# Optimization experiments

Measured on AMD Instinct MI355X. Metric: run time of the kernel, lower is better.

Reference implementation:

```python
import jax, jax.numpy as jnp
import numpy as np
import math

T, P, L, C, H, NPTS = 243, 17, 4, 128, 8, 4
DH = C // H


def _ln(x, g, b):
    m = jnp.mean(x, axis=-1, keepdims=True)
    v = jnp.mean((x - m) ** 2, axis=-1, keepdims=True)
    return (x - m) * jax.lax.rsqrt(v + 1e-5) * g + b


def _bilinear(v, grid):
    # v: [B, D, Hh, Ww]; grid: [B, Q, Pt, 2] in [-1,1], (x->W, y->H),
    # align_corners=False, zero padding (matches F.grid_sample in MSDeformAttn core)
    B, D, Hh, Ww = v.shape
    x = (grid[..., 0] + 1.0) * (Ww * 0.5) - 0.5
    y = (grid[..., 1] + 1.0) * (Hh * 0.5) - 0.5
    x0 = jnp.floor(x)
    y0 = jnp.floor(y)
    x0i = x0.astype(jnp.int32)
    y0i = y0.astype(jnp.int32)
    x1i = x0i + 1
    y1i = y0i + 1
    wx1 = x - x0
    wx0 = 1.0 - wx1
    wy1 = y - y0
    wy0 = 1.0 - wy1
    vf = v.reshape(B, D, Hh * Ww)
    Q, Pt = x.shape[1], x.shape[2]

    def gather(yi, xi):
        valid = ((yi >= 0) & (yi < Hh) & (xi >= 0) & (xi < Ww)).astype(v.dtype)
        idx = jnp.clip(yi, 0, Hh - 1) * Ww + jnp.clip(xi, 0, Ww - 1)
        g = jnp.take_along_axis(vf, idx.reshape(B, 1, Q * Pt), axis=2).reshape(B, D, Q, Pt)
        return g * valid[:, None]

    return (gather(y0i, x0i) * (wy0 * wx0)[:, None]
            + gather(y0i, x1i) * (wy0 * wx1)[:, None]
            + gather(y1i, x0i) * (wy1 * wx0)[:, None]
            + gather(y1i, x1i) * (wy1 * wx1)[:, None])  # [B, D, Q, Pt]


def _forward(x, ref_points, pe_buf, learn_pos, w_off, b_off, w_attn, b_attn,
             w_val, b_val, w_out, b_out, in_w, in_b, out_w, out_b,
             fc1_w, fc1_b, fc2_w, fc2_b, g1, be1, g2, be2, g3, be3):
    b, t, p, l, c = x.shape  # l = n_levels + 1
    Lq = t * p * L
    x0 = x[..., :1, :]
    xs = x[..., 1:, :].reshape(b, Lq, c)
    # --- subforward_self: norm_1 -> PE(query) -> MSDeformAttn ---
    xn = _ln(xs, g1, be1)
    q = (xn.reshape(b, t, p, L, c) + pe_buf + learn_pos).reshape(b, Lq, c)
    off = (q @ w_off.T + b_off).reshape(b, Lq, H, L, NPTS, 2)
    aw = jax.nn.softmax((q @ w_attn.T + b_attn).reshape(b, Lq, H, L * NPTS), axis=-1)
    aw = aw.reshape(b, Lq, H, L, NPTS)
    ref = jnp.broadcast_to(ref_points[:, :, :, None, :], (b, t, p, L, 2)).reshape(b, Lq, 2)
    normalizer = jnp.array([p, t], dtype=x.dtype)  # (W, H) per level
    loc = ref[:, :, None, None, None, :] + off / normalizer  # [b,Lq,H,L,Pt,2]
    grids = 2.0 * loc - 1.0
    val = (xn @ w_val.T + b_val).reshape(b, t, p, L, H, DH)
    v_maps = val.transpose(3, 0, 4, 5, 1, 2).reshape(L, b * H, DH, t, p)
    g = grids.transpose(3, 0, 2, 1, 4, 5).reshape(L, b * H, Lq, NPTS, 2)
    sampled = jax.vmap(_bilinear)(v_maps, g)  # [L, b*H, DH, Lq, Pt]
    aw_t = aw.transpose(3, 0, 2, 1, 4).reshape(L, b * H, 1, Lq, NPTS)
    o = jnp.sum(sampled * aw_t, axis=(0, 4))  # [b*H, DH, Lq]
    o = o.reshape(b, H, DH, Lq).transpose(0, 3, 1, 2).reshape(b, Lq, c)
    xs = (o @ w_out.T + b_out) + xs
    # --- concat level-0 back, cross (self) MHA over (p*l) tokens per frame ---
    xcat = jnp.concatenate([x0, xs.reshape(b, t, p, L, c)], axis=3).reshape(b * t, p * l, c)
    xn2 = _ln(xcat, g2, be2)
    qkv = xn2 @ in_w.T + in_b
    qh, kh, vh = jnp.split(qkv, 3, axis=-1)
    S = p * l
    qh = qh.reshape(b * t, S, H, DH)
    kh = kh.reshape(b * t, S, H, DH)
    vh = vh.reshape(b * t, S, H, DH)
    att = jax.nn.softmax(jnp.einsum('bqhd,bkhd->bhqk', qh, kh) / math.sqrt(DH), axis=-1)
    ca = jnp.einsum('bhqk,bkhd->bqhd', att, vh).reshape(b * t, S, c) @ out_w.T + out_b
    xcat = ca + xcat
    xr = xcat.reshape(b, t, p, l, c)
    # --- MLP block ---
    h = _ln(xr, g3, be3)
    h = jax.nn.gelu(h @ fc1_w.T + fc1_b, approximate=False) @ fc2_w.T + fc2_b
    return h + xr


def setup_inputs() -> dict:
    key = jax.random.key(0)
    ks = jax.random.split(key, 20)
    B = 2
    s = 0.02
    x = jax.random.normal(ks[0], (B, T, P, L + 1, C), jnp.float32)
    ref_points = jax.random.uniform(ks[1], (B, T, P, 2), dtype=jnp.float32)
    # sinusoidal PE buffer
    pos = np.arange(T, dtype=np.float32)[:, None]
    div = np.exp(np.arange(0, C, 2, dtype=np.float32) * (-math.log(10000.0) / C))
    ang = pos * div  # [T, C//2]
    pe = np.zeros((1, T, P, L, C), np.float32)
    pe[..., 0::2] = np.sin(ang)[None, :, None, None, :]
    pe[..., 1::2] = np.cos(ang)[None, :, None, None, :]
    rn = lambda k, shp: s * jax.random.normal(k, shp, jnp.float32)
    return {
        'x': x, 'ref_points': ref_points,
        'pe_buf': jnp.asarray(pe),
        'learn_pos': rn(ks[2], (1, T, P, L, C)),
        'w_off': rn(ks[3], (H * L * NPTS * 2, C)), 'b_off': rn(ks[4], (H * L * NPTS * 2,)),
        'w_attn': rn(ks[5], (H * L * NPTS, C)), 'b_attn': rn(ks[6], (H * L * NPTS,)),
        'w_val': rn(ks[7], (C, C)), 'b_val': rn(ks[8], (C,)),
        'w_out': rn(ks[9], (C, C)), 'b_out': rn(ks[10], (C,)),
        'in_w': rn(ks[11], (3 * C, C)), 'in_b': rn(ks[12], (3 * C,)),
        'out_w': rn(ks[13], (C, C)), 'out_b': rn(ks[14], (C,)),
        'fc1_w': rn(ks[15], (4 * C, C)), 'fc1_b': rn(ks[16], (4 * C,)),
        'fc2_w': rn(ks[17], (C, 4 * C)), 'fc2_b': rn(ks[18], (C,)),
        'g1': jnp.ones((C,), jnp.float32), 'be1': jnp.zeros((C,), jnp.float32),
        'g2': jnp.ones((C,), jnp.float32), 'be2': jnp.zeros((C,), jnp.float32),
        'g3': jnp.ones((C,), jnp.float32), 'be3': jnp.zeros((C,), jnp.float32),
    }


def reference(x, ref_points, pe_buf, learn_pos, w_off, b_off, w_attn, b_attn,
              w_val, b_val, w_out, b_out, in_w, in_b, out_w, out_b,
              fc1_w, fc1_b, fc2_w, fc2_b, g1, be1, g2, be2, g3, be3):
    return _forward(x, ref_points, pe_buf, learn_pos, w_off, b_off, w_attn, b_attn,
                    w_val, b_val, w_out, b_out, in_w, in_b, out_w, out_b,
                    fc1_w, fc1_b, fc2_w, fc2_b, g1, be1, g2, be2, g3, be3)
```

## Files before the change

kernel.cpp:

```cpp
#include <hip/hip_runtime.h>
#include <math.h>

#define T_ 243
#define P_ 17
#define L_ 4
#define C_ 128
#define H_ 8
#define NPTS_ 4
#define DH_ 16
#define B_ 2
#define LQ (T_*P_*L_)
#define NT1 (B_*LQ)
#define LL (L_+1)
#define S_ (P_*LL)
#define NT2 (B_*T_*P_*LL)

typedef __attribute__((ext_vector_type(8))) short short8v;
typedef __attribute__((ext_vector_type(4))) short short4v;
typedef __attribute__((ext_vector_type(4))) float float4v;

__device__ __forceinline__ unsigned short f2bf(float f){
  union { float f; unsigned u; } un; un.f = f;
  unsigned r = un.u + 0x7FFF + ((un.u >> 16) & 1);
  return (unsigned short)(r >> 16);
}
__device__ __forceinline__ float bf2f(unsigned short u){
  union { unsigned u; float f; } un; un.u = ((unsigned)u) << 16; return un.f;
}
__device__ __forceinline__ void dma16(const unsigned short* g, unsigned short* l){
  __builtin_amdgcn_global_load_lds(
      (const __attribute__((address_space(1))) void*)g,
      (__attribute__((address_space(3))) void*)l, 16, 0, 0);
}

__global__ void k_wcvt(const float* __restrict__ w0, const float* __restrict__ w1,
                       const float* __restrict__ w2, const float* __restrict__ w3,
                       const float* __restrict__ w4, const float* __restrict__ w5,
                       const float* __restrict__ w6, const float* __restrict__ w7,
                       unsigned short* __restrict__ dst){
  int i = blockIdx.x*256 + threadIdx.x;
  if (i >= 278528) return;
  float v;
  if      (i < 32768)  v = w0[i];
  else if (i < 49152)  v = w1[i-32768];
  else if (i < 65536)  v = w2[i-49152];
  else if (i < 81920)  v = w3[i-65536];
  else if (i < 131072) v = w4[i-81920];
  else if (i < 147456) v = w5[i-131072];
  else if (i < 212992) v = w6[i-147456];
  else                 v = w7[i-212992];
  dst[i] = f2bf(v);
}

__global__ __launch_bounds__(256) void k_ln1_q(
    const float* __restrict__ x, const float* __restrict__ pe,
    const float* __restrict__ lpos, const float* __restrict__ g1,
    const float* __restrict__ be1, const float* __restrict__ g2,
    const float* __restrict__ be2, unsigned short* __restrict__ xn,
    unsigned short* __restrict__ q, float* __restrict__ xcat,
    unsigned short* __restrict__ xn2) {
  int w = threadIdx.x >> 6; int lane = threadIdx.x & 63;
  int i = blockIdx.x*4 + w;
  int c = lane*2;
  if (i < NT1){
    int b = i / LQ; int r = i % LQ;
    int t = r / (P_*L_); int rp = r % (P_*L_);
    int p = rp / L_; int lv = rp % L_;
    const float* xrow = x + (((size_t)(b*T_+t)*P_ + p)*LL + 1 + lv)*C_;
    float2 v = *(const float2*)(xrow + c);
    float s1 = v.x + v.y, s2 = v.x*v.x + v.y*v.y;
    #pragma unroll
    for (int d=1; d<64; d<<=1){ s1 += __shfl_xor(s1,d); s2 += __shfl_xor(s2,d); }
    float mean = s1*(1.0f/C_);
    float var  = s2*(1.0f/C_) - mean*mean;
    float inv = rsqrtf(var + 1e-5f);
    float2 gg = *(const float2*)(g1 + c);
    float2 bb = *(const float2*)(be1 + c);
    float xn0 = (v.x - mean)*inv*gg.x + bb.x;
    float xn1 = (v.y - mean)*inv*gg.y + bb.y;
    size_t oi = (size_t)i*C_ + c;
    *(unsigned*)(xn + oi) = (unsigned)f2bf(xn0) | ((unsigned)f2bf(xn1) << 16);
    size_t pidx = (((size_t)t*P_ + p)*L_ + lv)*C_ + c;
    float2 pv = *(const float2*)(pe + pidx);
    float2 lp = *(const float2*)(lpos + pidx);
    *(unsigned*)(q + oi) = (unsigned)f2bf(xn0 + pv.x + lp.x) | ((unsigned)f2bf(xn1 + pv.y + lp.y) << 16);
  } else {
    int i0 = i - NT1;
    if (i0 >= B_*T_*P_) return;
    size_t xrow = (size_t)i0*LL;
    const float* xr = x + xrow*C_;
    float2 v = *(const float2*)(xr + c);
    float s1 = v.x + v.y, s2 = v.x*v.x + v.y*v.y;
    #pragma unroll
    for (int d=1; d<64; d<<=1){ s1 += __shfl_xor(s1,d); s2 += __shfl_xor(s2,d); }
    float mean = s1*(1.0f/C_);
    float var  = s2*(1.0f/C_) - mean*mean;
    float inv = rsqrtf(var + 1e-5f);
    float2 gg = *(const float2*)(g2 + c);
    float2 bb = *(const float2*)(be2 + c);
    *(float2*)(xcat + xrow*C_ + c) = v;
    float o0 = (v.x - mean)*inv*gg.x + bb.x;
    float o1 = (v.y - mean)*inv*gg.y + bb.y;
    *(unsigned*)(xn2 + xrow*C_ + c) = (unsigned)f2bf(o0) | ((unsigned)f2bf(o1) << 16);
  }
}

template<int K, int N, int EPI>
__global__ __launch_bounds__(256) void k_mm(
    const unsigned short* __restrict__ A, const unsigned short* __restrict__ Bw,
    const float* __restrict__ bias, const float* __restrict__ res,
    float* __restrict__ outF, unsigned short* __restrict__ outB,
    const float* __restrict__ xres, const float* __restrict__ lng,
    const float* __restrict__ lnbe, int M)
{
  constexpr int NST = K / 128;
  __shared__ unsigned short As[64*128];
  __shared__ unsigned short Bs[128*128];
  int tid = threadIdx.x;
  int lane = tid & 63;
  int w = tid >> 6;
  int lr = lane & 15, kg = lane >> 4;
  int m0 = blockIdx.x * 64;
  int n0 = blockIdx.y * 128;
  int lrow = lane >> 4;
  int lch  = lane & 15;
  float4v acc[8] = {};
  for (int st = 0; st < NST; ++st){
    int kk = st*128;
    if (st) __syncthreads();
    #pragma unroll
    for (int j = 0; j < 4; ++j){
      int rb = w*16 + j*4;
      int srcch = lch ^ ((rb + lrow) & 7);
      dma16(A + (size_t)(m0 + rb + lrow)*K + kk + srcch*8, As + rb*128);
    }
    #pragma unroll
    for (int j = 0; j < 8; ++j){
      int rb = w*32 + j*4;
      int srcch = lch ^ ((rb + lrow) & 7);
      dma16(Bw + (size_t)(n0 + rb + lrow)*K + kk + srcch*8, Bs + rb*128);
    }
    __syncthreads();
    #pragma unroll
    for (int ks = 0; ks < 4; ++ks){
      int cn = ks*4 + kg;
      int arow = w*16 + lr;
      short8v af = *(const short8v*)(As + arow*128 + ((cn ^ (arow & 7)) * 8));
      #pragma unroll
      for (int nf = 0; nf < 8; ++nf){
        int brow = nf*16 + lr;
        short8v bf = *(const short8v*)(Bs + brow*128 + ((cn ^ (brow & 7)) * 8));
        acc[nf] = __builtin_amdgcn_mfma_f32_16x16x32_bf16(af, bf, acc[nf], 0, 0, 0);
      }
    }
  }
  #pragma unroll
  for (int j = 0; j < 4; ++j){
    int gr = m0 + w*16 + kg*4 + j;
    if (gr >= M) continue;
    if (EPI == 3 || EPI == 4 || EPI == 5){
      #pragma unroll
      for (int nf = 0; nf < 8; ++nf){
        int gc = n0 + nf*16 + lr;
        float v = acc[nf][j] + bias[gc];
        if (EPI == 3) {
          outF[(size_t)gr*N + gc] = v + res[(size_t)gr*N + gc];
        } else if (EPI == 4) {
          float gv = 0.5f*v*(1.0f + erff(v*0.70710678118654752440f));
          outB[(size_t)gr*N + gc] = f2bf(gv);
        } else {
          outB[(size_t)gr*N + gc] = f2bf(v);
        }
      }
    } else {
      size_t xrow;
      if (EPI == 6){
        int b = gr / LQ; int r = gr % LQ;
        int t = r / (P_*L_); int rp = r % (P_*L_);
        int p = rp / L_; int lv = rp % L_;
        xrow = (((size_t)(b*T_+t)*P_ + p)*LL) + 1 + lv;
      } else {
        xrow = (size_t)gr;
      }
      float vals[8];
      float s = 0.f, sq = 0.f;
      #pragma unroll
      for (int nf = 0; nf < 8; ++nf){
        int gc = n0 + nf*16 + lr;
        float v = acc[nf][j] + bias[gc];
        if (EPI == 6) v += xres[xrow*C_ + gc];
        else          v += res[xrow*C_ + gc];
        vals[nf] = v; s += v; sq += v*v;
      }
      #pragma unroll
      for (int d = 1; d < 16; d <<= 1){ s += __shfl_xor(s, d); sq += __shfl_xor(sq, d); }
      float mean = s*(1.0f/128.f);
      float varr = sq*(1.0f/128.f) - mean*mean;
      float linv = rsqrtf(varr + 1e-5f);
      #pragma unroll
      for (int nf = 0; nf < 8; ++nf){
        int gc = n0 + nf*16 + lr;
        outF[xrow*C_ + gc] = vals[nf];
        float ln = (vals[nf] - mean)*linv*lng[gc] + lnbe[gc];
        outB[xrow*C_ + gc] = f2bf(ln);
      }
    }
  }
}

__global__ __launch_bounds__(256) void k_mm3(
    const unsigned short* __restrict__ Aq, const unsigned short* __restrict__ Axn,
    const unsigned short* __restrict__ Bw,
    const float* __restrict__ b_off, const float* __restrict__ b_attn,
    const float* __restrict__ b_val,
    unsigned short* __restrict__ off_b, unsigned short* __restrict__ aw_b,
    unsigned short* __restrict__ vm_b, int M)
{
  __shared__ unsigned short As[64*128];
  __shared__ unsigned short Bs[128*128];
  int tid = threadIdx.x;
  int lane = tid & 63;
  int w = tid >> 6;
  int lr = lane & 15, kg = lane >> 4;
  int m0 = blockIdx.x * 64;
  int y  = blockIdx.y;
  int n0 = y * 128;
  const unsigned short* A = (y == 3) ? Axn : Aq;
  int lrow = lane >> 4;
  int lch  = lane & 15;
  float4v acc[8] = {};
  #pragma unroll
  for (int j = 0; j < 4; ++j){
    int rb = w*16 + j*4;
    int srcch = lch ^ ((rb + lrow) & 7);
    dma16(A + (size_t)(m0 + rb + lrow)*128 + srcch*8, As + rb*128);
  }
  #pragma unroll
  for (int j = 0; j < 8; ++j){
    int rb = w*32 + j*4;
    int srcch = lch ^ ((rb + lrow) & 7);
    dma16(Bw + (size_t)(n0 + rb + lrow)*128 + srcch*8, Bs + rb*128);
  }
  __syncthreads();
  #pragma unroll
  for (int ks = 0; ks < 4; ++ks){
    int cn = ks*4 + kg;
    int arow = w*16 + lr;
    short8v af = *(const short8v*)(As + arow*128 + ((cn ^ (arow & 7)) * 8));
    #pragma unroll
    for (int nf = 0; nf < 8; ++nf){
      int brow = nf*16 + lr;
      short8v bf = *(const short8v*)(Bs + brow*128 + ((cn ^ (brow & 7)) * 8));
      acc[nf] = __builtin_amdgcn_mfma_f32_16x16x32_bf16(af, bf, acc[nf], 0, 0, 0);
    }
  }
  const float* bias = (y < 2) ? b_off : (y == 2 ? b_attn - 256 : b_val - 384);
  #pragma unroll
  for (int j = 0; j < 4; ++j){
    int gr = m0 + w*16 + kg*4 + j;
    if (gr >= M) continue;
    #pragma unroll
    for (int nf = 0; nf < 8; ++nf){
      int gc = n0 + nf*16 + lr;
      float v = acc[nf][j] + bias[gc];
      unsigned short bv = f2bf(v);
      if (y < 2)      off_b[(size_t)gr*256 + gc]       = bv;
      else if (y==2)  aw_b [(size_t)gr*128 + gc - 256] = bv;
      else            vm_b [(size_t)gr*128 + gc - 384] = bv;
    }
  }
}

__global__ __launch_bounds__(256) void k_sample(
    const unsigned short* __restrict__ off, const unsigned short* __restrict__ awl,
    const float* __restrict__ refp, const unsigned short* __restrict__ vmap,
    unsigned short* __restrict__ o){
  int gid = blockIdx.x*256 + threadIdx.x;
  if (gid >= NT1*H_) return;
  int h = gid & 7; int i = gid >> 3;
  int b = i / LQ; int r = i % LQ;
  int t = r/(P_*L_); int rp = r%(P_*L_); int p = rp/L_;
  size_t rpi = (((size_t)b*T_+t)*P_+p)*2;
  float refx = refp[rpi + 0]*P_ - 0.5f;
  float refy = refp[rpi + 1]*T_ - 0.5f;

  float offv[32];
  {
    const short8v* op8 = (const short8v*)(off + (size_t)i*256 + h*32);
    #pragma unroll
    for (int s=0;s<4;++s){ short8v v = op8[s];
      #pragma unroll
      for (int j=0;j<8;++j) offv[s*8+j] = bf2f((unsigned short)v[j]); }
  }
  float awv[16];
  {
    const short8v* ap8 = (const short8v*)(awl + (size_t)i*128 + h*16);
    #pragma unroll
    for (int s=0;s<2;++s){ short8v v = ap8[s];
      #pragma unroll
      for (int j=0;j<8;++j) awv[s*8+j] = bf2f((unsigned short)v[j]); }
  }
  float m = awv[0];
  #pragma unroll
  for (int k=1;k<16;++k) m = fmaxf(m, awv[k]);
  float sum = 0.f;
  #pragma unroll
  for (int k=0;k<16;++k){ awv[k] = __expf(awv[k]-m); sum += awv[k]; }
  float inv = 1.f/sum;
  #pragma unroll
  for (int k=0;k<16;++k) awv[k] *= inv;

  float acc[16];
  #pragma unroll
  for (int d=0;d<16;++d) acc[d]=0.f;

  #pragma unroll
  for (int lv=0; lv<L_; ++lv){
    const unsigned short* vlv = vmap + ((size_t)b*LQ + lv)*128 + h*16;
    #pragma unroll
    for (int pt=0; pt<NPTS_; ++pt){
      float px = refx + offv[(lv*4+pt)*2+0];
      float py = refy + offv[(lv*4+pt)*2+1];
      float w  = awv[lv*4+pt];
      float fx = floorf(px), fy = floorf(py);
      int x0 = (int)fx, y0 = (int)fy;
      float wx1 = px - fx, wx0 = 1.f - wx1;
      float wy1 = py - fy, wy0 = 1.f - wy1;
      float cw[4] = {w*wy0*wx0, w*wy0*wx1, w*wy1*wx0, w*wy1*wx1};
      int ys[4] = {y0, y0, y0+1, y0+1};
      int xs[4] = {x0, x0+1, x0, x0+1};
      #pragma unroll
      for (int cidx=0; cidx<4; ++cidx){
        int yy = ys[cidx], xx = xs[cidx];
        if (yy>=0 && yy<T_ && xx>=0 && xx<P_){
          const short8v* vp = (const short8v*)(vlv + (size_t)(yy*P_ + xx)*(L_*128));
          short8v v0 = vp[0], v1 = vp[1];
          float wgt = cw[cidx];
          #pragma unroll
          for (int d=0;d<8;++d){
            acc[d]   = fmaf(wgt, bf2f((unsigned short)v0[d]), acc[d]);
            acc[8+d] = fmaf(wgt, bf2f((unsigned short)v1[d]), acc[8+d]);
          }
        }
      }
    }
  }
  short8v o0, o1;
  #pragma unroll
  for (int d=0;d<8;++d){ o0[d] = (short)f2bf(acc[d]); o1[d] = (short)f2bf(acc[8+d]); }
  short8v* op = (short8v*)(o + (size_t)i*C_ + h*DH_);
  op[0] = o0; op[1] = o1;
}

#define AT6_WAVE 6976
__global__ __launch_bounds__(128) void k_attn6(const unsigned short* __restrict__ qkv,
                                               unsigned short* __restrict__ ca){
  __shared__ unsigned short alds[2*AT6_WAVE];
  int w = threadIdx.x >> 6; int lane = threadIdx.x & 63;
  int bt = blockIdx.x >> 2; int hp = blockIdx.x & 3;
  int h = hp*2 + w;
  unsigned short* Kb  = alds + w*AT6_WAVE;
  unsigned short* Vb  = Kb + 1920;
  unsigned short* Pb0 = Kb + 3648;
  unsigned short* Pb1 = Kb + 5312;
  const unsigned short* base = qkv + (size_t)bt*85*384 + h*16;
  for (int idx = lane; idx < 192; idx += 64){
    int s = idx >> 1; int d0 = (idx & 1)*8;
    short8v kv = {}, vv = {};
    if (s < 85){
      const unsigned short* rp = base + (size_t)s*384 + d0;
      kv = *(const short8v*)(rp + 128);
      vv = *(const short8v*)(rp + 256);
    }
    *(short8v*)(Kb + s*20 + d0) = kv;
    #pragma unroll
    for (int j=0;j<8;++j) Vb[(d0+j)*108 + s] = (unsigned short)vv[j];
  }
  __syncthreads();
  int g = lane >> 4; int li = lane & 15;
  const short8v zero8 = {};
  short8v qf0 = zero8, qf1 = zero8;
  if (g < 2){
    if (li < 85) qf0 = *(const short8v*)(base + (size_t)li*384 + g*8);
    int q1i = 16 + li;
    if (q1i < 85) qf1 = *(const short8v*)(base + (size_t)q1i*384 + g*8);
  }
  #pragma unroll 1
  for (int qp = 0; qp < 3; ++qp){
    short8v qn0 = zero8, qn1 = zero8;
    if (qp < 2 && g < 2){
      int a = (qp+1)*32 + li, b2 = a + 16;
      if (a  < 85) qn0 = *(const short8v*)(base + (size_t)a *384 + g*8);
      if (b2 < 85) qn1 = *(const short8v*)(base + (size_t)b2*384 + g*8);
    }
    float4v sc0[6], sc1[6];
    __builtin_amdgcn_s_setprio(1);
    #pragma unroll
    for (int kt = 0; kt < 6; ++kt){
      short8v kf = zero8;
      if (g < 2) kf = *(const short8v*)(Kb + (kt*16 + li)*20 + g*8);
      float4v z = {};
      sc0[kt] = __builtin_amdgcn_mfma_f32_16x16x32_bf16(kf, qf0, z, 0, 0, 0);
      sc1[kt] = __builtin_amdgcn_mfma_f32_16x16x32_bf16(kf, qf1, z, 0, 0, 0);
    }
    __builtin_amdgcn_s_setprio(0);
    float sum0 = 0.f, sum1 = 0.f;
    #pragma unroll
    for (int kt = 0; kt < 6; ++kt){
      short4v p0, p1;
      #pragma unroll
      for (int j = 0; j < 4; ++j){
        bool msk = (kt == 5 && (g*4 + j) >= 5);
        float e0 = msk ? 0.f : __expf(sc0[kt][j]*0.25f);
        float e1 = msk ? 0.f : __expf(sc1[kt][j]*0.25f);
        sum0 += e0; p0[j] = (short)f2bf(e0);
        sum1 += e1; p1[j] = (short)f2bf(e1);
      }
      *(short4v*)(Pb0 + li*104 + kt*16 + g*4) = p0;
      *(short4v*)(Pb1 + li*104 + kt*16 + g*4) = p1;
    }
    sum0 += __shfl_xor(sum0, 16); sum1 += __shfl_xor(sum1, 16);
    sum0 += __shfl_xor(sum0, 32); sum1 += __shfl_xor(sum1, 32);
    float inv0 = 1.f/sum0, inv1 = 1.f/sum1;
    float4v o0 = {}, o1 = {};
    __builtin_amdgcn_s_setprio(1);
    #pragma unroll
    for (int kt32 = 0; kt32 < 3; ++kt32){
      short8v vf  = *(const short8v*)(Vb  + li*108 + kt32*32 + g*8);
      short8v p80 = *(const short8v*)(Pb0 + li*104 + kt32*32 + g*8);
      short8v p81 = *(const short8v*)(Pb1 + li*104 + kt32*32 + g*8);
      o0 = __builtin_amdgcn_mfma_f32_16x16x32_bf16(vf, p80, o0, 0, 0, 0);
      o1 = __builtin_amdgcn_mfma_f32_16x16x32_bf16(vf, p81, o1, 0, 0, 0);
    }
    __builtin_amdgcn_s_setprio(0);
    int q0 = qp*32 + li, q1 = q0 + 16;
    if (q0 < 85){
      short4v ov;
      #pragma unroll
      for (int j=0;j<4;++j) ov[j] = (short)f2bf(o0[j]*inv0);
      *(short4v*)(ca + ((size_t)bt*85 + q0)*128 + h*16 + g*4) = ov;
    }
    if (q1 < 85){
      short4v ov;
      #pragma unroll
      for (int j=0;j<4;++j) ov[j] = (short)f2bf(o1[j]*inv1);
      *(short4v*)(ca + ((size_t)bt*85 + q1)*128 + h*16 + g*4) = ov;
    }
    qf0 = qn0; qf1 = qn1;
  }
}

extern "C" void kernel_launch(void* const* d_in, const int* in_sizes, int n_in,
                              void* d_out, int out_size, void* d_ws, size_t ws_size,
                              hipStream_t stream) {
  (void)in_sizes; (void)n_in; (void)out_size; (void)ws_size;
  const float* x      = (const float*)d_in[0];
  const float* refp   = (const float*)d_in[1];
  const float* pe     = (const float*)d_in[2];
  const float* lpos   = (const float*)d_in[3];
  const float* w_off  = (const float*)d_in[4];
  const float* b_off  = (const float*)d_in[5];
  const float* w_attn = (const float*)d_in[6];
  const float* b_attn = (const float*)d_in[7];
  const float* w_val  = (const float*)d_in[8];
  const float* b_val  = (const float*)d_in[9];
  const float* w_out  = (const float*)d_in[10];
  const float* b_out  = (const float*)d_in[11];
  const float* in_w   = (const float*)d_in[12];
  const float* in_b   = (const float*)d_in[13];
  const float* out_w  = (const float*)d_in[14];
  const float* out_b  = (const float*)d_in[15];
  const float* fc1_w  = (const float*)d_in[16];
  const float* fc1_b  = (const float*)d_in[17];
  const float* fc2_w  = (const float*)d_in[18];
  const float* fc2_b  = (const float*)d_in[19];
  const float* g1     = (const float*)d_in[20];
  const float* be1    = (const float*)d_in[21];
  const float* g2     = (const float*)d_in[22];
  const float* be2    = (const float*)d_in[23];
  const float* g3     = (const float*)d_in[24];
  const float* be3    = (const float*)d_in[25];
  float* out = (float*)d_out;
  char* wsb = (char*)d_ws;

  unsigned short* xn_b  = (unsigned short*)(wsb + 0);
  unsigned short* q_b   = (unsigned short*)(wsb + 8460288);
  unsigned short* off_b = (unsigned short*)(wsb + 16920576);
  unsigned short* aw_b  = (unsigned short*)(wsb + 33841152);
  unsigned short* vm_b  = (unsigned short*)(wsb + 42301440);
  unsigned short* o_b   = (unsigned short*)(wsb + 50761728);
  float*          xcatB = (float*)(wsb + 59222016);
  unsigned short* xn2_b = (unsigned short*)(wsb + 80372736);
  unsigned short* qkv_b = (unsigned short*)(wsb + 90948096);
  unsigned short* wb    = (unsigned short*)(wsb + 122674176);
  unsigned short* ca_b  = (unsigned short*)(wsb + 0);
  unsigned short* ln3_b = (unsigned short*)(wsb + 80372736);
  unsigned short* hid_b = (unsigned short*)(wsb + 16920576);

  unsigned short* wb_off  = wb + 0;
  unsigned short* wb_wout = wb + 65536;
  unsigned short* wb_in   = wb + 81920;
  unsigned short* wb_outw = wb + 131072;
  unsigned short* wb_fc1  = wb + 147456;
  unsigned short* wb_fc2  = wb + 212992;

  const int GM1 = (NT1 + 63)/64;
  const int GM2 = (NT2 + 63)/64;

  hipLaunchKernelGGL(k_wcvt, dim3((278528+255)/256), dim3(256), 0, stream,
                     w_off, w_attn, w_val, w_out, in_w, out_w, fc1_w, fc2_w, wb);
  hipLaunchKernelGGL(k_ln1_q, dim3((NT1 + B_*T_*P_ + 3)/4), dim3(256), 0, stream,
                     x, pe, lpos, g1, be1, g2, be2, xn_b, q_b, xcatB, xn2_b);
  hipLaunchKernelGGL(k_mm3, dim3(GM1,4), dim3(256), 0, stream,
                     q_b, xn_b, wb_off, b_off, b_attn, b_val, off_b, aw_b, vm_b, NT1);
  hipLaunchKernelGGL(k_sample, dim3((NT1*H_+255)/256), dim3(256), 0, stream,
                     off_b, aw_b, refp, vm_b, o_b);
  hipLaunchKernelGGL((k_mm<128,128,6>), dim3(GM1,1), dim3(256), 0, stream,
                     o_b, wb_wout, b_out, nullptr, xcatB, xn2_b, x, g2, be2, NT1);
  hipLaunchKernelGGL((k_mm<128,384,5>), dim3(GM2,3), dim3(256), 0, stream,
                     xn2_b, wb_in, in_b, nullptr, nullptr, qkv_b, nullptr, nullptr, nullptr, NT2);
  hipLaunchKernelGGL(k_attn6, dim3(B_*T_*4), dim3(128), 0, stream, qkv_b, ca_b);
  hipLaunchKernelGGL((k_mm<128,128,7>), dim3(GM2,1), dim3(256), 0, stream,
                     ca_b, wb_outw, out_b, xcatB, xcatB, ln3_b, nullptr, g3, be3, NT2);
  hipLaunchKernelGGL((k_mm<128,512,4>), dim3(GM2,4), dim3(256), 0, stream,
                     ln3_b, wb_fc1, fc1_b, nullptr, nullptr, hid_b, nullptr, nullptr, nullptr, NT2);
  hipLaunchKernelGGL((k_mm<512,128,3>), dim3(GM2,1), dim3(256), 0, stream,
                     hid_b, wb_fc2, fc2_b, xcatB, out, nullptr, nullptr, nullptr, nullptr, NT2);
}
```

Before: 204.5 us.

## Split deformable sampling across two threads per head and remap blocks per XCD

Result: slower. 211.9 us (+3.6%).

```diff
diff --git a/kernel.cpp b/kernel.cpp
--- a/kernel.cpp
+++ b/kernel.cpp
@@ -271,13 +271,18 @@
   }
 }
 
+#define SMP_N (NT1*H_*2)
+#define SMP_B ((SMP_N + 255)/256)
 __global__ __launch_bounds__(256) void k_sample(
     const unsigned short* __restrict__ off, const unsigned short* __restrict__ awl,
     const float* __restrict__ refp, const unsigned short* __restrict__ vmap,
     unsigned short* __restrict__ o){
-  int gid = blockIdx.x*256 + threadIdx.x;
-  if (gid >= NT1*H_) return;
-  int h = gid & 7; int i = gid >> 3;
+  const int nB = SMP_B, q8 = nB >> 3, r8 = nB & 7;
+  int xcd = blockIdx.x & 7, idx8 = blockIdx.x >> 3;
+  int lb = (xcd < r8) ? xcd*(q8+1) + idx8 : r8*(q8+1) + (xcd - r8)*q8 + idx8;
+  int gid = lb*256 + threadIdx.x;
+  if (gid >= SMP_N) return;
+  int half = gid & 1; int hh = (gid >> 1) & 7; int i = gid >> 4;
   int b = i / LQ; int r = i % LQ;
   int t = r/(P_*L_); int rp = r%(P_*L_); int p = rp/L_;
   size_t rpi = (((size_t)b*T_+t)*P_+p)*2;
@@ -286,7 +291,7 @@
 
   float offv[32];
   {
-    const short8v* op8 = (const short8v*)(off + (size_t)i*256 + h*32);
+    const short8v* op8 = (const short8v*)(off + (size_t)i*256 + hh*32);
     #pragma unroll
     for (int s=0;s<4;++s){ short8v v = op8[s];
       #pragma unroll
@@ -294,7 +299,7 @@
   }
   float awv[16];
   {
-    const short8v* ap8 = (const short8v*)(awl + (size_t)i*128 + h*16);
+    const short8v* ap8 = (const short8v*)(awl + (size_t)i*128 + hh*16);
     #pragma unroll
     for (int s=0;s<2;++s){ short8v v = ap8[s];
       #pragma unroll
@@ -310,13 +315,13 @@
   #pragma unroll
   for (int k=0;k<16;++k) awv[k] *= inv;
 
-  float acc[16];
-  #pragma unroll
-  for (int d=0;d<16;++d) acc[d]=0.f;
+  float acc[8];
+  #pragma unroll
+  for (int d=0;d<8;++d) acc[d]=0.f;
 
   #pragma unroll
   for (int lv=0; lv<L_; ++lv){
-    const unsigned short* vlv = vmap + ((size_t)b*LQ + lv)*128 + h*16;
+    const unsigned short* vlv = vmap + ((size_t)b*LQ + lv)*128 + hh*16 + half*8;
     #pragma unroll
     for (int pt=0; pt<NPTS_; ++pt){
       float px = refx + offv[(lv*4+pt)*2+0];
@@ -333,23 +338,19 @@
       for (int cidx=0; cidx<4; ++cidx){
         int yy = ys[cidx], xx = xs[cidx];
         if (yy>=0 && yy<T_ && xx>=0 && xx<P_){
-          const short8v* vp = (const short8v*)(vlv + (size_t)(yy*P_ + xx)*(L_*128));
-          short8v v0 = vp[0], v1 = vp[1];
+          short8v v0 = *(const short8v*)(vlv + (size_t)(yy*P_ + xx)*(L_*128));
           float wgt = cw[cidx];
           #pragma unroll
-          for (int d=0;d<8;++d){
-            acc[d]   = fmaf(wgt, bf2f((unsigned short)v0[d]), acc[d]);
-            acc[8+d] = fmaf(wgt, bf2f((unsigned short)v1[d]), acc[8+d]);
-          }
+          for (int d=0;d<8;++d)
+            acc[d] = fmaf(wgt, bf2f((unsigned short)v0[d]), acc[d]);
         }
       }
     }
   }
-  short8v o0, o1;
-  #pragma unroll
-  for (int d=0;d<8;++d){ o0[d] = (short)f2bf(acc[d]); o1[d] = (short)f2bf(acc[8+d]); }
-  short8v* op = (short8v*)(o + (size_t)i*C_ + h*DH_);
-  op[0] = o0; op[1] = o1;
+  short8v o0;
+  #pragma unroll
+  for (int d=0;d<8;++d) o0[d] = (short)f2bf(acc[d]);
+  *(short8v*)(o + (size_t)i*C_ + hh*DH_ + half*8) = o0;
 }
 
 #define AT6_WAVE 6976
@@ -513,7 +514,7 @@
                      x, pe, lpos, g1, be1, g2, be2, xn_b, q_b, xcatB, xn2_b);
   hipLaunchKernelGGL(k_mm3, dim3(GM1,4), dim3(256), 0, stream,
                      q_b, xn_b, wb_off, b_off, b_attn, b_val, off_b, aw_b, vm_b, NT1);
-  hipLaunchKernelGGL(k_sample, dim3((NT1*H_+255)/256), dim3(256), 0, stream,
+  hipLaunchKernelGGL(k_sample, dim3(SMP_B), dim3(256), 0, stream,
                      off_b, aw_b, refp, vm_b, o_b);
   hipLaunchKernelGGL((k_mm<128,128,6>), dim3(GM1,1), dim3(256), 0, stream,
                      o_b, wb_wout, b_out, nullptr, xcatB, xn2_b, x, g2, be2, NT1);
```

## Keep attention probabilities in registers using 16x16x16 MFMA for PV product

Applied to the files above, without the earlier changes.

Result: faster. 199.0 us (-2.7%).

```diff
diff --git a/kernel.cpp b/kernel.cpp
--- a/kernel.cpp
+++ b/kernel.cpp
@@ -18,6 +18,12 @@
 typedef __attribute__((ext_vector_type(8))) short short8v;
 typedef __attribute__((ext_vector_type(4))) short short4v;
 typedef __attribute__((ext_vector_type(4))) float float4v;
+
+#if defined(__has_builtin)
+# if __has_builtin(__builtin_amdgcn_mfma_f32_16x16x16bf16_1k)
+#  define HAVE_M16 1
+# endif
+#endif
 
 __device__ __forceinline__ unsigned short f2bf(float f){
   union { float f; unsigned u; } un; un.f = f;
@@ -352,17 +358,23 @@
   op[0] = o0; op[1] = o1;
 }
 
-#define AT6_WAVE 6976
-__global__ __launch_bounds__(128) void k_attn6(const unsigned short* __restrict__ qkv,
+#ifdef HAVE_M16
+#define AT7_WAVE 3648
+#else
+#define AT7_WAVE 6976
+#endif
+__global__ __launch_bounds__(128) void k_attn7(const unsigned short* __restrict__ qkv,
                                                unsigned short* __restrict__ ca){
-  __shared__ unsigned short alds[2*AT6_WAVE];
+  __shared__ unsigned short alds[2*AT7_WAVE];
   int w = threadIdx.x >> 6; int lane = threadIdx.x & 63;
   int bt = blockIdx.x >> 2; int hp = blockIdx.x & 3;
   int h = hp*2 + w;
-  unsigned short* Kb  = alds + w*AT6_WAVE;
+  unsigned short* Kb  = alds + w*AT7_WAVE;
   unsigned short* Vb  = Kb + 1920;
+#ifndef HAVE_M16
   unsigned short* Pb0 = Kb + 3648;
   unsigned short* Pb1 = Kb + 5312;
+#endif
   const unsigned short* base = qkv + (size_t)bt*85*384 + h*16;
   for (int idx = lane; idx < 192; idx += 64){
     int s = idx >> 1; int d0 = (idx & 1)*8;
@@ -405,6 +417,8 @@
     }
     __builtin_amdgcn_s_setprio(0);
     float sum0 = 0.f, sum1 = 0.f;
+    float4v o0 = {}, o1 = {};
+#ifdef HAVE_M16
     #pragma unroll
     for (int kt = 0; kt < 6; ++kt){
       short4v p0, p1;
@@ -416,14 +430,25 @@
         sum0 += e0; p0[j] = (short)f2bf(e0);
         sum1 += e1; p1[j] = (short)f2bf(e1);
       }
+      short4v vf = *(const short4v*)(Vb + li*108 + kt*16 + g*4);
+      o0 = __builtin_amdgcn_mfma_f32_16x16x16bf16_1k(vf, p0, o0, 0, 0, 0);
+      o1 = __builtin_amdgcn_mfma_f32_16x16x16bf16_1k(vf, p1, o1, 0, 0, 0);
+    }
+#else
+    #pragma unroll
+    for (int kt = 0; kt < 6; ++kt){
+      short4v p0, p1;
+      #pragma unroll
+      for (int j = 0; j < 4; ++j){
+        bool msk = (kt == 5 && (g*4 + j) >= 5);
+        float e0 = msk ? 0.f : __expf(sc0[kt][j]*0.25f);
+        float e1 = msk ? 0.f : __expf(sc1[kt][j]*0.25f);
+        sum0 += e0; p0[j] = (short)f2bf(e0);
+        sum1 += e1; p1[j] = (short)f2bf(e1);
+      }
       *(short4v*)(Pb0 + li*104 + kt*16 + g*4) = p0;
       *(short4v*)(Pb1 + li*104 + kt*16 + g*4) = p1;
     }
-    sum0 += __shfl_xor(sum0, 16); sum1 += __shfl_xor(sum1, 16);
-    sum0 += __shfl_xor(sum0, 32); sum1 += __shfl_xor(sum1, 32);
-    float inv0 = 1.f/sum0, inv1 = 1.f/sum1;
-    float4v o0 = {}, o1 = {};
-    __builtin_amdgcn_s_setprio(1);
     #pragma unroll
     for (int kt32 = 0; kt32 < 3; ++kt32){
       short8v vf  = *(const short8v*)(Vb  + li*108 + kt32*32 + g*8);
@@ -432,7 +457,10 @@
       o0 = __builtin_amdgcn_mfma_f32_16x16x32_bf16(vf, p80, o0, 0, 0, 0);
       o1 = __builtin_amdgcn_mfma_f32_16x16x32_bf16(vf, p81, o1, 0, 0, 0);
     }
-    __builtin_amdgcn_s_setprio(0);
+#endif
+    sum0 += __shfl_xor(sum0, 16); sum1 += __shfl_xor(sum1, 16);
+    sum0 += __shfl_xor(sum0, 32); sum1 += __shfl_xor(sum1, 32);
+    float inv0 = 1.f/sum0, inv1 = 1.f/sum1;
     int q0 = qp*32 + li, q1 = q0 + 16;
     if (q0 < 85){
       short4v ov;
@@ -519,7 +547,7 @@
                      o_b, wb_wout, b_out, nullptr, xcatB, xn2_b, x, g2, be2, NT1);
   hipLaunchKernelGGL((k_mm<128,384,5>), dim3(GM2,3), dim3(256), 0, stream,
                      xn2_b, wb_in, in_b, nullptr, nullptr, qkv_b, nullptr, nullptr, nullptr, NT2);
-  hipLaunchKernelGGL(k_attn6, dim3(B_*T_*4), dim3(128), 0, stream, qkv_b, ca_b);
+  hipLaunchKernelGGL(k_attn7, dim3(B_*T_*4), dim3(128), 0, stream, qkv_b, ca_b);
   hipLaunchKernelGGL((k_mm<128,128,7>), dim3(GM2,1), dim3(256), 0, stream,
                      ca_b, wb_outw, out_b, xcatB, xcatB, ln3_b, nullptr, g3, be3, NT2);
   hipLaunchKernelGGL((k_mm<128,512,4>), dim3(GM2,4), dim3(256), 0, stream,
```
